# Performance work log

Hardware: AMD Instinct MI355X
Metric: run time of the kernel (lower is better)

Reference implementation:

```python
import jax, jax.numpy as jnp
import numpy as np

B, L, D, H, LIN = 256, 128, 1024, 512, 512


def _lstm_masked(xs, lengths, W_ih, W_hh, b):
    # xs: [L, B, D] time-major. Emulates pack_padded_sequence: state frozen and
    # output zeroed for t >= length (pad_packed pads with zeros).
    nb = xs.shape[1]
    hdim = W_hh.shape[1]

    def step(carry, inp):
        h, c = carry
        xt, t = inp
        g = xt @ W_ih.T + h @ W_hh.T + b  # [B, 4H], gate order i,f,g,o (PyTorch)
        i, f, gg, o = jnp.split(g, 4, axis=-1)
        i = jax.nn.sigmoid(i)
        f = jax.nn.sigmoid(f)
        gg = jnp.tanh(gg)
        o = jax.nn.sigmoid(o)
        c_new = f * c + i * gg
        h_new = o * jnp.tanh(c_new)
        valid = (t < lengths)[:, None]
        h2 = jnp.where(valid, h_new, h)
        c2 = jnp.where(valid, c_new, c)
        out = jnp.where(valid, h_new, 0.0)
        return (h2, c2), out

    init = (jnp.zeros((nb, hdim), xs.dtype), jnp.zeros((nb, hdim), xs.dtype))
    ts = jnp.arange(xs.shape[0])
    _, outs = jax.lax.scan(step, init, (xs, ts))
    return outs  # [L, B, H]


def _reverse_valid(x, lengths):
    # Reverse each sequence within its valid prefix, zero the tail. x: [B, L, F]
    t = jnp.arange(x.shape[1])
    idx = jnp.clip(lengths[:, None] - 1 - t[None, :], 0, x.shape[1] - 1)
    g = jnp.take_along_axis(x, idx[:, :, None], axis=1)
    mask = (t[None, :] < lengths[:, None])[:, :, None]
    return jnp.where(mask, g, 0.0)


def setup_inputs() -> dict:
    key = jax.random.key(0)
    ks = jax.random.split(key, 16)
    s = 0.05
    x_len = jax.random.randint(ks[2], (B,), L // 2, L + 1, dtype=jnp.int32).at[0].set(L)
    return {
        "x": jax.random.normal(ks[0], (B, 1, L, D), jnp.float32),
        "x_len": x_len,
        "epoch": 1,
        "target_word": jax.random.normal(ks[1], (B, 1, 5, D), jnp.float32),
        "tokens": jax.random.randint(ks[3], (B, L), 0, 30000, dtype=jnp.int32),
        "W_ih_f": jax.random.normal(ks[4], (4 * H, D), jnp.float32) * s,
        "W_hh_f": jax.random.normal(ks[5], (4 * H, H), jnp.float32) * s,
        "b_f": jnp.zeros((4 * H,), jnp.float32),
        "W_ih_b": jax.random.normal(ks[6], (4 * H, D), jnp.float32) * s,
        "W_hh_b": jax.random.normal(ks[7], (4 * H, H), jnp.float32) * s,
        "b_b": jnp.zeros((4 * H,), jnp.float32),
        "W_h": jax.random.uniform(ks[8], (2 * D, 1), jnp.float32),
        "b_tanh": jax.random.uniform(ks[9], (L,), jnp.float32),
        "W_lin": jax.random.normal(ks[10], (LIN, 2 * H), jnp.float32) * s,
        "b_lin": jnp.zeros((LIN,), jnp.float32),
        "W_out": jax.random.normal(ks[11], (3, LIN), jnp.float32) * s,
        "b_out": jnp.zeros((3,), jnp.float32),
    }


def reference(x, x_len, epoch, target_word, tokens,
              W_ih_f, W_hh_f, b_f, W_ih_b, W_hh_b, b_b,
              W_h, b_tanh, W_lin, b_lin, W_out, b_out):
    xe = x[:, 0]                         # [B, L, D]
    tw = target_word[:, 0].mean(axis=1)  # [B, D] (sum/size == mean)
    lengths = x_len

    # Bidirectional LSTM with length masking (packed-sequence semantics)
    out_f = _lstm_masked(xe.transpose(1, 0, 2), lengths, W_ih_f, W_hh_f, b_f).transpose(1, 0, 2)
    x_rev = _reverse_valid(xe, lengths)
    out_b_rev = _lstm_masked(x_rev.transpose(1, 0, 2), lengths, W_ih_b, W_hh_b, b_b).transpose(1, 0, 2)
    out_b = _reverse_valid(out_b_rev, lengths)
    h_lstm = jnp.concatenate([out_f, out_b], axis=-1)  # [B, L, 2H]

    # Additive attention score: concat(xe, tw) @ W_h, decomposed (same math)
    u = jnp.einsum('bld,d->bl', xe, W_h[:D, 0]) + (tw @ W_h[D:, 0])[:, None] + b_tanh[None, :]
    mask = jnp.arange(L)[None, :] < lengths[:, None]
    u = jnp.where(mask, u, -1e6)
    alphas = jax.nn.softmax(u, axis=1)
    context = jnp.einsum('bl,blh->bh', alphas, h_lstm)  # [B, 2H]

    lin = jax.nn.relu(context @ W_lin.T + b_lin)
    return lin @ W_out.T + b_out
```

## Files before the change

### kernel.cpp

```cpp
#include <hip/hip_runtime.h>
#include <cstdint>
#include <cstddef>

typedef unsigned short u16;
typedef unsigned long long ull;
typedef __attribute__((ext_vector_type(8))) short bf16x8;
typedef __attribute__((ext_vector_type(4))) float f32x4;

#define NB 256
#define LL 128
#define DD 1024
#define HH 512
#define GG 2048
#define NN 4096
#define LINN 512

__device__ __forceinline__ u16 f2bf(float f) {
  unsigned u = __float_as_uint(f);
  u += 0x7fffu + ((u >> 16) & 1u);
  return (u16)(u >> 16);
}
__device__ __forceinline__ float sigm(float x) { return 1.0f / (1.0f + __expf(-x)); }
__device__ __forceinline__ float tanh_fast(float x) {
  float a = fabsf(x);
  float e = __expf(-2.0f * a);
  float t = (1.0f - e) / (1.0f + e);
  return copysignf(t, x);
}
__device__ __forceinline__ void load_lds16(const void* g, void* l) {
  __builtin_amdgcn_global_load_lds(
      (const __attribute__((address_space(1))) void*)g,
      (__attribute__((address_space(3))) void*)l, 16, 0, 0);
}

__global__ __launch_bounds__(256) void conv_bf16(const float* __restrict__ in,
                                                 u16* __restrict__ out) {
  size_t i = ((size_t)blockIdx.x * 256 + threadIdx.x) * 8;
  float4 a = *(const float4*)(in + i);
  float4 b = *(const float4*)(in + i + 4);
  uint4 v;
  v.x = (unsigned)f2bf(a.x) | ((unsigned)f2bf(a.y) << 16);
  v.y = (unsigned)f2bf(a.z) | ((unsigned)f2bf(a.w) << 16);
  v.z = (unsigned)f2bf(b.x) | ((unsigned)f2bf(b.y) << 16);
  v.w = (unsigned)f2bf(b.z) | ((unsigned)f2bf(b.w) << 16);
  *(uint4*)(out + i) = v;
}

__global__ __launch_bounds__(256) void prep_weights(
    const float* __restrict__ Wih_f, const float* __restrict__ Whh_f, const float* __restrict__ b_f,
    const float* __restrict__ Wih_b, const float* __restrict__ Whh_b, const float* __restrict__ b_b,
    u16* __restrict__ Wih_p, u16* __restrict__ Whh_p, float* __restrict__ bias_p) {
  int idx = blockIdx.x * 256 + threadIdx.x;
  int p = idx >> 10, k = idx & 1023;
  int src = ((p & 3) << 9) | (p >> 2);
  Wih_p[(size_t)p * DD + k] = f2bf(Wih_f[(size_t)src * DD + k]);
  Wih_p[(size_t)GG * DD + (size_t)p * DD + k] = f2bf(Wih_b[(size_t)src * DD + k]);
  if (k < HH) {
    Whh_p[(size_t)p * HH + k] = f2bf(Whh_f[(size_t)src * HH + k]);
    Whh_p[(size_t)GG * HH + (size_t)p * HH + k] = f2bf(Whh_b[(size_t)src * HH + k]);
  }
  if (k == 0) { bias_p[p] = b_f[src]; bias_p[GG + p] = b_b[src]; }
}

__global__ __launch_bounds__(256) void attn_alpha(
    const float* __restrict__ x, const float* __restrict__ tword,
    const float* __restrict__ W_h, const float* __restrict__ b_tanh,
    const int* __restrict__ xlen, float* __restrict__ alpha) {
  int b = blockIdx.x, tid = threadIdx.x;
  int lane = tid & 63, wave = tid >> 6;
  __shared__ float wred[4];
  __shared__ float uvals[LL];
  const float* tw = tword + (size_t)b * 5 * DD;
  float acc = 0.f;
  for (int i = tid; i < 5 * DD; i += 256) acc += tw[i] * W_h[DD + (i & (DD - 1))];
  #pragma unroll
  for (int off = 32; off; off >>= 1) acc += __shfl_down(acc, off);
  if (lane == 0) wred[wave] = acc;
  __syncthreads();
  float twdot = (wred[0] + wred[1] + wred[2] + wred[3]) * 0.2f;
  int len = xlen[b];
  const float* xb = x + (size_t)b * LL * DD;
  for (int l = wave; l < LL; l += 4) {
    float s = 0.f;
    if (l < len) {
      const float* xr = xb + (size_t)l * DD;
      for (int k = lane * 4; k < DD; k += 256) {
        float4 xv = *(const float4*)(xr + k);
        float4 wv = *(const float4*)(W_h + k);
        s += xv.x * wv.x + xv.y * wv.y + xv.z * wv.z + xv.w * wv.w;
      }
      #pragma unroll
      for (int off = 32; off; off >>= 1) s += __shfl_down(s, off);
    }
    if (lane == 0) uvals[l] = (l < len) ? (s + twdot + b_tanh[l]) : -1000000.0f;
  }
  __syncthreads();
  if (wave == 0) {
    float u0 = uvals[lane], u1 = uvals[lane + 64];
    float m = fmaxf(u0, u1);
    #pragma unroll
    for (int off = 32; off; off >>= 1) m = fmaxf(m, __shfl_down(m, off));
    m = __shfl(m, 0);
    float e0 = __expf(u0 - m), e1 = __expf(u1 - m);
    float ssum = e0 + e1;
    #pragma unroll
    for (int off = 32; off; off >>= 1) ssum += __shfl_down(ssum, off);
    ssum = __shfl(ssum, 0);
    alpha[(size_t)b * LL + lane] = e0 / ssum;
    alpha[(size_t)b * LL + lane + 64] = e1 / ssum;
  }
}

__global__ __launch_bounds__(256) void gemm_bt(
    const u16* __restrict__ A, const u16* __restrict__ Bw, u16* __restrict__ C) {
  __shared__ u16 At[128 * 64];
  __shared__ u16 Bt[128 * 64];
  const int tid = threadIdx.x;
  const int lane = tid & 63, wave = tid >> 6;
  const int m0 = blockIdx.y * 128, n0 = blockIdx.x * 128;
  const int wm = (wave >> 1) * 64, wn = (wave & 1) * 64;
  const int l15 = lane & 15, quad = lane >> 4;
  f32x4 acc[4][4] = {};
  const int rs = tid >> 3;
  const int slot = tid & 7;
  for (int kt = 0; kt < 16; ++kt) {
    __syncthreads();
    #pragma unroll
    for (int cc = 0; cc < 4; ++cc) {
      int row = cc * 32 + rs;
      int kseg = slot ^ (row & 7);
      const u16* ga = A + (size_t)(m0 + row) * DD + kt * 64 + kseg * 8;
      const u16* gb = Bw + (size_t)(n0 + row) * DD + kt * 64 + kseg * 8;
      load_lds16(ga, (char*)At + cc * 4096 + tid * 16);
      load_lds16(gb, (char*)Bt + cc * 4096 + tid * 16);
    }
    __syncthreads();
    #pragma unroll
    for (int ks = 0; ks < 2; ++ks) {
      bf16x8 av[4], bv[4];
      int kq = ks * 4 + quad;
      #pragma unroll
      for (int i = 0; i < 4; ++i) {
        int row = wm + i * 16 + l15;
        av[i] = *(const bf16x8*)(At + row * 64 + (kq ^ (row & 7)) * 8);
      }
      #pragma unroll
      for (int j = 0; j < 4; ++j) {
        int row = wn + j * 16 + l15;
        bv[j] = *(const bf16x8*)(Bt + row * 64 + (kq ^ (row & 7)) * 8);
      }
      #pragma unroll
      for (int i = 0; i < 4; ++i)
        #pragma unroll
        for (int j = 0; j < 4; ++j)
          acc[i][j] = __builtin_amdgcn_mfma_f32_16x16x32_bf16(av[i], bv[j], acc[i][j], 0, 0, 0);
    }
  }
  #pragma unroll
  for (int i = 0; i < 4; ++i) {
    #pragma unroll
    for (int r = 0; r < 4; ++r) {
      size_t row = (size_t)(m0 + wm + i * 16 + quad * 4 + r);
      u16* crow = C + row * NN + n0 + wn + l15;
      #pragma unroll
      for (int j = 0; j < 4; ++j) crow[j * 16] = f2bf(acc[i][j][r]);
    }
  }
}

__global__ __launch_bounds__(256, 1) void lstm_persist(
    const u16* __restrict__ P, const u16* __restrict__ Whh_p,
    const float* __restrict__ bias_p, const float* __restrict__ alpha,
    const int* __restrict__ xlen, u16* __restrict__ hfrag,
    float* __restrict__ ctx, int* __restrict__ bar, unsigned* __restrict__ xmask) {
  __shared__ u16 Wl[128 * 512];
  __shared__ float gbuf[32][132];
  __shared__ float biasl[128];
  __shared__ int xl[32];
  __shared__ unsigned same_sh;
  const int tid = threadIdx.x;
  const int lane = tid & 63, wave = tid >> 6;
  const int l15 = lane & 15, quad = lane >> 4;
  const int bid = blockIdx.x;
  const int gid = bid & 15;
  const int ncol = bid >> 4;
  const int dir = gid >> 3, btile = gid & 7;

  {
    const u16* Wb = Whh_p + ((size_t)dir * GG + ncol * 128) * HH;
    for (int idx = tid; idx < 128 * 64; idx += 256) {
      int row = idx >> 6, seg = idx & 63;
      int sseg = seg ^ (row & 7);
      *(uint4*)&Wl[row * 512 + sseg * 8] = *(const uint4*)(Wb + (size_t)row * HH + seg * 8);
    }
  }
  if (tid < 128) biasl[tid] = bias_p[(size_t)dir * GG + ncol * 128 + tid];
  if (tid < 32) xl[tid] = xlen[btile * 32 + tid];

  unsigned xcc;
  asm volatile("s_getreg_b32 %0, hwreg(HW_REG_XCC_ID)" : "=s"(xcc));
  if (tid == 0) {
    __hip_atomic_fetch_or(&xmask[gid], 1u << (xcc & 31), __ATOMIC_RELAXED,
                          __HIP_MEMORY_SCOPE_AGENT);
    __builtin_amdgcn_fence(__ATOMIC_RELEASE, "agent");
    int* c = bar + ((size_t)gid * (LL + 1) + LL) * 32;
    __hip_atomic_fetch_add(c, 1, __ATOMIC_RELAXED, __HIP_MEMORY_SCOPE_AGENT);
    while (__hip_atomic_load(c, __ATOMIC_RELAXED, __HIP_MEMORY_SCOPE_AGENT) < 16)
      __builtin_amdgcn_s_sleep(1);
    __builtin_amdgcn_fence(__ATOMIC_ACQUIRE, "agent");
    same_sh = (__popc(__hip_atomic_load(&xmask[gid], __ATOMIC_RELAXED,
                                        __HIP_MEMORY_SCOPE_AGENT)) == 1) ? 1u : 0u;
  }
  __syncthreads();
  const bool same_xcd = (same_sh != 0);

  const int b_local = tid >> 3, jb = tid & 7;
  const int b_glob = btile * 32 + b_local;
  const int jg0 = ncol * 32 + jb * 4;
  const size_t hslot = ((size_t)(dir * 64 + (jg0 >> 3)) * 256 + b_glob) * 8 + (jg0 & 7);
  const int len = xl[b_local];

  float creg[4] = {0.f, 0.f, 0.f, 0.f};
  float ctxa[4] = {0.f, 0.f, 0.f, 0.f};
  u16 hv[4] = {0, 0, 0, 0};

  const int bt = wave >> 1, ch = wave & 1;
  const int b0 = btile * 32 + bt * 16;

  const u16* Pbase = P + (size_t)b_glob * LL * NN + (size_t)dir * GG + ncol * 128 + jb * 16;
  int t0 = dir ? (len - 1) : 0;
  t0 = min(max(t0, 0), LL - 1);
  uint4 pa = *(const uint4*)(Pbase + (size_t)t0 * NN);
  uint4 pb = *(const uint4*)(Pbase + (size_t)t0 * NN + 8);
  float al = alpha[(size_t)b_glob * LL + t0];

  const size_t HBUF = (size_t)2 * 64 * 256 * 8;
  for (int s = 0; s < LL; ++s) {
    const u16* hc = hfrag + (size_t)(s & 1) * HBUF;
    u16* hx = hfrag + (size_t)((s + 1) & 1) * HBUF;

    bf16x8 av[16];
    #pragma unroll
    for (int ks = 0; ks < 16; ++ks) {
      const ull* ap = (const ull*)(hc + ((size_t)(dir * 64 + ks * 4 + quad) * 256 + b0 + l15) * 8);
      union { ull q[2]; bf16x8 v; } u;
      u.q[0] = __hip_atomic_load(ap, __ATOMIC_RELAXED, __HIP_MEMORY_SCOPE_AGENT);
      u.q[1] = __hip_atomic_load(ap + 1, __ATOMIC_RELAXED, __HIP_MEMORY_SCOPE_AGENT);
      av[ks] = u.v;
    }
    f32x4 acc[4] = {};
    #pragma unroll
    for (int ks = 0; ks < 16; ++ks) {
      #pragma unroll
      for (int nt = 0; nt < 4; ++nt) {
        int r = ch * 64 + nt * 16 + l15;
        bf16x8 bv = *(const bf16x8*)&Wl[r * 512 + ((ks * 4 + quad) ^ (r & 7)) * 8];
        acc[nt] = __builtin_amdgcn_mfma_f32_16x16x32_bf16(av[ks], bv, acc[nt], 0, 0, 0);
      }
    }
    #pragma unroll
    for (int nt = 0; nt < 4; ++nt)
      #pragma unroll
      for (int r = 0; r < 4; ++r)
        gbuf[bt * 16 + quad * 4 + r][ch * 64 + nt * 16 + l15] = acc[nt][r];
    __syncthreads();

    const bool valid = s < len;
    unsigned pw[8] = {pa.x, pa.y, pa.z, pa.w, pb.x, pb.y, pb.z, pb.w};
    #pragma unroll
    for (int u = 0; u < 4; ++u) {
      float4 gv = *(const float4*)&gbuf[b_local][jb * 16 + u * 4];
      float4 bb = *(const float4*)&biasl[jb * 16 + u * 4];
      float gi = gv.x + __uint_as_float(pw[u * 2] << 16) + bb.x;
      float gf = gv.y + __uint_as_float(pw[u * 2] & 0xffff0000u) + bb.y;
      float gz = gv.z + __uint_as_float(pw[u * 2 + 1] << 16) + bb.z;
      float go = gv.w + __uint_as_float(pw[u * 2 + 1] & 0xffff0000u) + bb.w;
      float ig = sigm(gi), fg = sigm(gf), zg = tanh_fast(gz), og = sigm(go);
      float cn = fg * creg[u] + ig * zg;
      float hn = og * tanh_fast(cn);
      if (valid) {
        creg[u] = cn;
        ctxa[u] += al * hn;
        hv[u] = f2bf(hn);
      }
    }
    *(ushort4*)&hx[hslot] = make_ushort4(hv[0], hv[1], hv[2], hv[3]);

    int tn = dir ? (len - 2 - s) : (s + 1);
    tn = min(max(tn, 0), LL - 1);
    uint4 npa = *(const uint4*)(Pbase + (size_t)tn * NN);
    uint4 npb = *(const uint4*)(Pbase + (size_t)tn * NN + 8);
    float nal = alpha[(size_t)b_glob * LL + tn];

    if (s < LL - 1) {
      __syncthreads();
      if (tid == 0) {
        int* c = bar + ((size_t)gid * (LL + 1) + s) * 32;
        if (same_xcd) {
          __hip_atomic_fetch_add(c, 1, __ATOMIC_RELAXED, __HIP_MEMORY_SCOPE_AGENT);
          while (__hip_atomic_load(c, __ATOMIC_RELAXED, __HIP_MEMORY_SCOPE_AGENT) < 16)
            ;
          __builtin_amdgcn_fence(__ATOMIC_ACQUIRE, "workgroup");
        } else {
          __builtin_amdgcn_fence(__ATOMIC_RELEASE, "agent");
          __hip_atomic_fetch_add(c, 1, __ATOMIC_RELAXED, __HIP_MEMORY_SCOPE_AGENT);
          while (__hip_atomic_load(c, __ATOMIC_RELAXED, __HIP_MEMORY_SCOPE_AGENT) < 16)
            __builtin_amdgcn_s_sleep(1);
          __builtin_amdgcn_fence(__ATOMIC_ACQUIRE, "agent");
        }
      }
      __syncthreads();
    }
    pa = npa; pb = npb; al = nal;
  }

  #pragma unroll
  for (int u = 0; u < 4; ++u)
    ctx[(size_t)b_glob * (2 * HH) + dir * HH + jg0 + u] = ctxa[u];
}

__global__ __launch_bounds__(256) void head(
    const float* __restrict__ ctx, const float* __restrict__ W_lin,
    const float* __restrict__ b_lin, const float* __restrict__ W_out,
    const float* __restrict__ b_out, float* __restrict__ out) {
  int b = blockIdx.x, tid = threadIdx.x;
  __shared__ float cbuf[2 * HH];
  __shared__ float lbuf[LINN];
  *(float4*)&cbuf[tid * 4] = *(const float4*)&ctx[(size_t)b * (2 * HH) + tid * 4];
  __syncthreads();
  #pragma unroll
  for (int rr = 0; rr < 2; ++rr) {
    int row = tid + rr * 256;
    const float* wr = W_lin + (size_t)row * (2 * HH);
    float s = 0.f;
    for (int k = 0; k < 2 * HH; k += 4) {
      float4 wv = *(const float4*)(wr + k);
      float4 cv = *(const float4*)(cbuf + k);
      s += wv.x * cv.x + wv.y * cv.y + wv.z * cv.z + wv.w * cv.w;
    }
    lbuf[row] = fmaxf(s + b_lin[row], 0.0f);
  }
  __syncthreads();
  int lane = tid & 63, wave = tid >> 6;
  if (wave < 3) {
    const float* wo = W_out + (size_t)wave * LINN;
    float s = 0.f;
    for (int k = lane; k < LINN; k += 64) s += lbuf[k] * wo[k];
    #pragma unroll
    for (int off = 32; off; off >>= 1) s += __shfl_down(s, off);
    if (lane == 0) out[(size_t)b * 3 + wave] = s + b_out[wave];
  }
}

extern "C" void kernel_launch(void* const* d_in, const int* in_sizes, int n_in,
                              void* d_out, int out_size, void* d_ws, size_t ws_size,
                              hipStream_t stream) {
  (void)in_sizes; (void)n_in; (void)out_size; (void)ws_size;
  const float* x      = (const float*)d_in[0];
  const int*   xlen   = (const int*)d_in[1];
  const float* tword  = (const float*)d_in[3];
  const float* Wih_f  = (const float*)d_in[5];
  const float* Whh_f  = (const float*)d_in[6];
  const float* b_f    = (const float*)d_in[7];
  const float* Wih_b  = (const float*)d_in[8];
  const float* Whh_b  = (const float*)d_in[9];
  const float* b_b    = (const float*)d_in[10];
  const float* W_h    = (const float*)d_in[11];
  const float* b_tanh = (const float*)d_in[12];
  const float* W_lin  = (const float*)d_in[13];
  const float* b_lin  = (const float*)d_in[14];
  const float* W_out  = (const float*)d_in[15];
  const float* b_out  = (const float*)d_in[16];
  float* out = (float*)d_out;

  char* w = (char*)d_ws;
  u16* xe_bf = (u16*)w;      w += (size_t)NB * LL * DD * 2;
  u16* Pbuf  = (u16*)w;      w += (size_t)NB * LL * NN * 2;
  u16* Wih_p = (u16*)w;      w += (size_t)2 * GG * DD * 2;
  u16* Whh_p = (u16*)w;      w += (size_t)2 * GG * HH * 2;
  float* bias_p = (float*)w; w += (size_t)2 * GG * 4;
  float* alphaW = (float*)w; w += (size_t)NB * LL * 4;
  u16* hfrag = (u16*)w;      w += (size_t)2 * 2 * 64 * 256 * 8 * 2;
  float* ctxb = (float*)w;   w += (size_t)NB * 2 * HH * 4;
  int* barW  = (int*)w;      w += (size_t)16 * (LL + 1) * 32 * 4;
  unsigned* xmaskW = (unsigned*)w; w += 16 * 4;

  hipMemsetAsync(hfrag, 0, (size_t)2 * 64 * 256 * 8 * 2, stream);
  hipMemsetAsync(barW, 0, (size_t)16 * (LL + 1) * 32 * 4, stream);
  hipMemsetAsync(xmaskW, 0, 16 * 4, stream);

  conv_bf16<<<16384, 256, 0, stream>>>(x, xe_bf);
  prep_weights<<<8192, 256, 0, stream>>>(Wih_f, Whh_f, b_f, Wih_b, Whh_b, b_b,
                                         Wih_p, Whh_p, bias_p);
  attn_alpha<<<256, 256, 0, stream>>>(x, tword, W_h, b_tanh, xlen, alphaW);
  gemm_bt<<<dim3(32, 256), 256, 0, stream>>>(xe_bf, Wih_p, Pbuf);

  {
    const u16* Pc = Pbuf;
    const u16* Wc = Whh_p;
    const float* bc = bias_p;
    const float* ac = alphaW;
    const int* lc = xlen;
    u16* hc = hfrag;
    float* cc = ctxb;
    int* brc = barW;
    unsigned* xm = xmaskW;
    void* kargs[] = {&Pc, &Wc, &bc, &ac, &lc, &hc, &cc, &brc, &xm};
    hipLaunchCooperativeKernel((const void*)lstm_persist, dim3(256), dim3(256),
                               kargs, 0, stream);
  }

  head<<<256, 256, 0, stream>>>(ctxb, W_lin, b_lin, W_out, b_out, out);
}
```

Measured before the change: 1.307 ms.

## Keep recurrent weights in registers, stage h in LDS, use per-block flag barrier

Each wave now holds its 32-column slice of W_hh in registers instead of reading it from LDS every step. The h state for the batch tile is staged once per step into shared memory and shared by all waves, replacing per-wave global atomic loads of A fragments. The gate buffer writes use a swizzle to cut LDS bank conflicts, and bias is kept in registers. When all blocks of a group sit on the same XCD, the atomic-counter barrier is replaced by per-block flag stores polled by 16 lanes. The cost is much higher register pressure and an extra __syncthreads per step.

Result: faster. 1.259 ms (-3.7%).

```diff
diff --git a/kernel.cpp b/kernel.cpp
--- a/kernel.cpp
+++ b/kernel.cpp
@@ -172,10 +172,10 @@
     const u16* __restrict__ P, const u16* __restrict__ Whh_p,
     const float* __restrict__ bias_p, const float* __restrict__ alpha,
     const int* __restrict__ xlen, u16* __restrict__ hfrag,
-    float* __restrict__ ctx, int* __restrict__ bar, unsigned* __restrict__ xmask) {
-  __shared__ u16 Wl[128 * 512];
+    float* __restrict__ ctx, int* __restrict__ bar,
+    unsigned* __restrict__ xmask, int* __restrict__ flags) {
+  __shared__ u16 Hs[64 * 32 * 8];
   __shared__ float gbuf[32][132];
-  __shared__ float biasl[128];
   __shared__ int xl[32];
   __shared__ unsigned same_sh;
   const int tid = threadIdx.x;
@@ -186,15 +186,15 @@
   const int ncol = bid >> 4;
   const int dir = gid >> 3, btile = gid & 7;
 
+  bf16x8 bw[2][16];
   {
-    const u16* Wb = Whh_p + ((size_t)dir * GG + ncol * 128) * HH;
-    for (int idx = tid; idx < 128 * 64; idx += 256) {
-      int row = idx >> 6, seg = idx & 63;
-      int sseg = seg ^ (row & 7);
-      *(uint4*)&Wl[row * 512 + sseg * 8] = *(const uint4*)(Wb + (size_t)row * HH + seg * 8);
-    }
-  }
-  if (tid < 128) biasl[tid] = bias_p[(size_t)dir * GG + ncol * 128 + tid];
+    const u16* Wb = Whh_p + ((size_t)dir * GG + ncol * 128 + wave * 32) * HH;
+    #pragma unroll
+    for (int nt = 0; nt < 2; ++nt)
+      #pragma unroll
+      for (int ks = 0; ks < 16; ++ks)
+        bw[nt][ks] = *(const bf16x8*)(Wb + (size_t)(nt * 16 + l15) * HH + ks * 32 + quad * 8);
+  }
   if (tid < 32) xl[tid] = xlen[btile * 32 + tid];
 
   unsigned xcc;
@@ -220,12 +220,14 @@
   const size_t hslot = ((size_t)(dir * 64 + (jg0 >> 3)) * 256 + b_glob) * 8 + (jg0 & 7);
   const int len = xl[b_local];
 
+  float4 bb[4];
+  #pragma unroll
+  for (int u = 0; u < 4; ++u)
+    bb[u] = *(const float4*)(bias_p + (size_t)dir * GG + ncol * 128 + jb * 16 + u * 4);
+
   float creg[4] = {0.f, 0.f, 0.f, 0.f};
   float ctxa[4] = {0.f, 0.f, 0.f, 0.f};
   u16 hv[4] = {0, 0, 0, 0};
-
-  const int bt = wave >> 1, ch = wave & 1;
-  const int b0 = btile * 32 + bt * 16;
 
   const u16* Pbase = P + (size_t)b_glob * LL * NN + (size_t)dir * GG + ncol * 128 + jb * 16;
   int t0 = dir ? (len - 1) : 0;
@@ -239,42 +241,50 @@
     const u16* hc = hfrag + (size_t)(s & 1) * HBUF;
     u16* hx = hfrag + (size_t)((s + 1) & 1) * HBUF;
 
-    bf16x8 av[16];
+    #pragma unroll
+    for (int i = 0; i < 8; ++i) {
+      int j = i * 256 + tid;
+      const ull* ap = (const ull*)(hc + ((size_t)(dir * 64 + (j >> 5)) * 256 + btile * 32 + (j & 31)) * 8);
+      union { ull q[2]; uint4 v; } un;
+      un.q[0] = __hip_atomic_load(ap, __ATOMIC_RELAXED, __HIP_MEMORY_SCOPE_AGENT);
+      un.q[1] = __hip_atomic_load(ap + 1, __ATOMIC_RELAXED, __HIP_MEMORY_SCOPE_AGENT);
+      *(uint4*)&Hs[(size_t)j * 8] = un.v;
+    }
+    __syncthreads();
+
+    f32x4 acc[2][2] = {};
     #pragma unroll
     for (int ks = 0; ks < 16; ++ks) {
-      const ull* ap = (const ull*)(hc + ((size_t)(dir * 64 + ks * 4 + quad) * 256 + b0 + l15) * 8);
-      union { ull q[2]; bf16x8 v; } u;
-      u.q[0] = __hip_atomic_load(ap, __ATOMIC_RELAXED, __HIP_MEMORY_SCOPE_AGENT);
-      u.q[1] = __hip_atomic_load(ap + 1, __ATOMIC_RELAXED, __HIP_MEMORY_SCOPE_AGENT);
-      av[ks] = u.v;
-    }
-    f32x4 acc[4] = {};
-    #pragma unroll
-    for (int ks = 0; ks < 16; ++ks) {
-      #pragma unroll
-      for (int nt = 0; nt < 4; ++nt) {
-        int r = ch * 64 + nt * 16 + l15;
-        bf16x8 bv = *(const bf16x8*)&Wl[r * 512 + ((ks * 4 + quad) ^ (r & 7)) * 8];
-        acc[nt] = __builtin_amdgcn_mfma_f32_16x16x32_bf16(av[ks], bv, acc[nt], 0, 0, 0);
-      }
-    }
-    #pragma unroll
-    for (int nt = 0; nt < 4; ++nt)
-      #pragma unroll
-      for (int r = 0; r < 4; ++r)
-        gbuf[bt * 16 + quad * 4 + r][ch * 64 + nt * 16 + l15] = acc[nt][r];
+      bf16x8 a0 = *(const bf16x8*)&Hs[(size_t)((ks * 4 + quad) * 32 + l15) * 8];
+      bf16x8 a1 = *(const bf16x8*)&Hs[(size_t)((ks * 4 + quad) * 32 + 16 + l15) * 8];
+      acc[0][0] = __builtin_amdgcn_mfma_f32_16x16x32_bf16(a0, bw[0][ks], acc[0][0], 0, 0, 0);
+      acc[0][1] = __builtin_amdgcn_mfma_f32_16x16x32_bf16(a0, bw[1][ks], acc[0][1], 0, 0, 0);
+      acc[1][0] = __builtin_amdgcn_mfma_f32_16x16x32_bf16(a1, bw[0][ks], acc[1][0], 0, 0, 0);
+      acc[1][1] = __builtin_amdgcn_mfma_f32_16x16x32_bf16(a1, bw[1][ks], acc[1][1], 0, 0, 0);
+    }
+    #pragma unroll
+    for (int mt = 0; mt < 2; ++mt)
+      #pragma unroll
+      for (int nt = 0; nt < 2; ++nt) {
+        int col = wave * 32 + nt * 16 + l15;
+        int jbw = col >> 4;
+        int swz = jbw * 16 + ((((col >> 2) & 3) + (jbw >> 1)) & 3) * 4 + (col & 3);
+        #pragma unroll
+        for (int r = 0; r < 4; ++r)
+          gbuf[mt * 16 + quad * 4 + r][swz] = acc[mt][nt][r];
+      }
     __syncthreads();
 
     const bool valid = s < len;
     unsigned pw[8] = {pa.x, pa.y, pa.z, pa.w, pb.x, pb.y, pb.z, pb.w};
     #pragma unroll
     for (int u = 0; u < 4; ++u) {
-      float4 gv = *(const float4*)&gbuf[b_local][jb * 16 + u * 4];
-      float4 bb = *(const float4*)&biasl[jb * 16 + u * 4];
-      float gi = gv.x + __uint_as_float(pw[u * 2] << 16) + bb.x;
-      float gf = gv.y + __uint_as_float(pw[u * 2] & 0xffff0000u) + bb.y;
-      float gz = gv.z + __uint_as_float(pw[u * 2 + 1] << 16) + bb.z;
-      float go = gv.w + __uint_as_float(pw[u * 2 + 1] & 0xffff0000u) + bb.w;
+      int cswz = jb * 16 + ((u + (jb >> 1)) & 3) * 4;
+      float4 gv = *(const float4*)&gbuf[b_local][cswz];
+      float gi = gv.x + __uint_as_float(pw[u * 2] << 16) + bb[u].x;
+      float gf = gv.y + __uint_as_float(pw[u * 2] & 0xffff0000u) + bb[u].y;
+      float gz = gv.z + __uint_as_float(pw[u * 2 + 1] << 16) + bb[u].z;
+      float go = gv.w + __uint_as_float(pw[u * 2 + 1] & 0xffff0000u) + bb[u].w;
       float ig = sigm(gi), fg = sigm(gf), zg = tanh_fast(gz), og = sigm(go);
       float cn = fg * creg[u] + ig * zg;
       float hn = og * tanh_fast(cn);
@@ -294,20 +304,22 @@
 
     if (s < LL - 1) {
       __syncthreads();
-      if (tid == 0) {
+      if (same_xcd) {
+        int* f = flags + ((size_t)gid * LL + s) * 16;
+        if (tid == 0)
+          __hip_atomic_store(&f[ncol], 1, __ATOMIC_RELAXED, __HIP_MEMORY_SCOPE_AGENT);
+        if (wave == 0 && lane < 16) {
+          while (__hip_atomic_load(&f[lane], __ATOMIC_RELAXED, __HIP_MEMORY_SCOPE_AGENT) == 0)
+            ;
+        }
+        __builtin_amdgcn_fence(__ATOMIC_ACQUIRE, "workgroup");
+      } else if (tid == 0) {
         int* c = bar + ((size_t)gid * (LL + 1) + s) * 32;
-        if (same_xcd) {
-          __hip_atomic_fetch_add(c, 1, __ATOMIC_RELAXED, __HIP_MEMORY_SCOPE_AGENT);
-          while (__hip_atomic_load(c, __ATOMIC_RELAXED, __HIP_MEMORY_SCOPE_AGENT) < 16)
-            ;
-          __builtin_amdgcn_fence(__ATOMIC_ACQUIRE, "workgroup");
-        } else {
-          __builtin_amdgcn_fence(__ATOMIC_RELEASE, "agent");
-          __hip_atomic_fetch_add(c, 1, __ATOMIC_RELAXED, __HIP_MEMORY_SCOPE_AGENT);
-          while (__hip_atomic_load(c, __ATOMIC_RELAXED, __HIP_MEMORY_SCOPE_AGENT) < 16)
-            __builtin_amdgcn_s_sleep(1);
-          __builtin_amdgcn_fence(__ATOMIC_ACQUIRE, "agent");
-        }
+        __builtin_amdgcn_fence(__ATOMIC_RELEASE, "agent");
+        __hip_atomic_fetch_add(c, 1, __ATOMIC_RELAXED, __HIP_MEMORY_SCOPE_AGENT);
+        while (__hip_atomic_load(c, __ATOMIC_RELAXED, __HIP_MEMORY_SCOPE_AGENT) < 16)
+          __builtin_amdgcn_s_sleep(1);
+        __builtin_amdgcn_fence(__ATOMIC_ACQUIRE, "agent");
       }
       __syncthreads();
     }
@@ -383,11 +395,13 @@
   u16* hfrag = (u16*)w;      w += (size_t)2 * 2 * 64 * 256 * 8 * 2;
   float* ctxb = (float*)w;   w += (size_t)NB * 2 * HH * 4;
   int* barW  = (int*)w;      w += (size_t)16 * (LL + 1) * 32 * 4;
-  unsigned* xmaskW = (unsigned*)w; w += 16 * 4;
-
-  hipMemsetAsync(hfrag, 0, (size_t)2 * 64 * 256 * 8 * 2, stream);
+  unsigned* xmaskW = (unsigned*)w; w += 64;
+  int* flagW = (int*)w;      w += (size_t)16 * LL * 16 * 4;
+
+  hipMemsetAsync(hfrag, 0, (size_t)2 * 2 * 64 * 256 * 8 * 2, stream);
   hipMemsetAsync(barW, 0, (size_t)16 * (LL + 1) * 32 * 4, stream);
-  hipMemsetAsync(xmaskW, 0, 16 * 4, stream);
+  hipMemsetAsync(xmaskW, 0, 64, stream);
+  hipMemsetAsync(flagW, 0, (size_t)16 * LL * 16 * 4, stream);
 
   conv_bf16<<<16384, 256, 0, stream>>>(x, xe_bf);
   prep_weights<<<8192, 256, 0, stream>>>(Wih_f, Whh_f, b_f, Wih_b, Whh_b, b_b,
@@ -405,7 +419,8 @@
     float* cc = ctxb;
     int* brc = barW;
     unsigned* xm = xmaskW;
-    void* kargs[] = {&Pc, &Wc, &bc, &ac, &lc, &hc, &cc, &brc, &xm};
+    int* fl = flagW;
+    void* kargs[] = {&Pc, &Wc, &bc, &ac, &lc, &hc, &cc, &brc, &xm, &fl};
     hipLaunchCooperativeKernel((const void*)lstm_persist, dim3(256), dim3(256),
                                kargs, 0, stream);
   }
```
